# Optimization experiments

Measured on AMD Instinct MI355X. Metric: run time of the kernel, lower is better.

The kernel has to match this reference:

```python
import jax, jax.numpy as jnp
import numpy as np

D_MODEL, D_STATE, D_CONV, EXPAND = 1024, 16, 4, 2
D_INNER = EXPAND * D_MODEL
BATCH, SEQ = 2, 2048


def setup_inputs() -> dict:
    key = jax.random.key(0)
    ks = jax.random.split(key, 10)
    s = lambda fan_in: 1.0 / np.sqrt(fan_in)
    return {
        "x": jax.random.normal(ks[0], (BATCH, SEQ, D_MODEL), jnp.float32),
        "W_in": jax.random.normal(ks[1], (2 * D_INNER, D_MODEL), jnp.float32) * s(D_MODEL),
        "w_conv": jax.random.normal(ks[2], (D_INNER, D_CONV), jnp.float32) * s(D_CONV),
        "b_conv": jax.random.normal(ks[3], (D_INNER,), jnp.float32) * 0.02,
        "W_x": jax.random.normal(ks[4], (D_INNER + 2 * D_STATE, D_INNER), jnp.float32) * s(D_INNER),
        "W_dt": jax.random.normal(ks[5], (D_INNER, D_INNER), jnp.float32) * s(D_INNER),
        "b_dt": jax.random.normal(ks[6], (D_INNER,), jnp.float32) * 0.02,
        "A_log": jnp.log(jax.random.uniform(ks[7], (D_INNER, D_STATE), jnp.float32, 1e-4, 1.0)),
        "D": jnp.ones((D_INNER,), jnp.float32),
        "W_out": jax.random.normal(ks[8], (D_MODEL, D_INNER), jnp.float32) * s(D_INNER),
    }


def _depthwise_causal_conv(x, w, b):
    # x: (B, L, C), w: (C, K), causal (left-pad K-1), matches conv1d(padding=K-1)[..., :L]
    K = w.shape[1]
    L = x.shape[1]
    xp = jnp.pad(x, ((0, 0), (K - 1, 0), (0, 0)))
    out = b
    for k in range(K):  # K is tiny (4)
        out = out + xp[:, k:k + L, :] * w[:, k]
    return out


def _selective_scan(x, delta, Bm, Cm, A, Dv):
    # x, delta: (B, L, d_inner); Bm, Cm: (B, L, d_state)
    def step(state, inp):
        x_t, d_t, B_t, C_t = inp  # (B,d_inner),(B,d_inner),(B,d_state),(B,d_state)
        decay = jnp.exp(d_t[..., None] * A)          # (B, d_inner, d_state)
        state = decay * state + B_t[:, None, :] * x_t[..., None]
        y_t = jnp.einsum('bds,bs->bd', state, C_t) + x_t * Dv
        return state, y_t

    init = jnp.zeros((x.shape[0], x.shape[2], A.shape[1]), x.dtype)
    xs = tuple(jnp.swapaxes(a, 0, 1) for a in (x, delta, Bm, Cm))
    _, ys = jax.lax.scan(step, init, xs)             # ys: (L, B, d_inner)
    return jnp.swapaxes(ys, 0, 1)


def reference(x, W_in, w_conv, b_conv, W_x, W_dt, b_dt, A_log, D, W_out):
    silu = jax.nn.silu
    xz = x @ W_in.T                                   # (B, L, 2*d_inner)
    x_inner, z = jnp.split(xz, 2, axis=-1)
    x_conv = silu(_depthwise_causal_conv(x_inner, w_conv, b_conv))
    x_dbl = x_conv @ W_x.T                            # (B, L, d_inner + 2*d_state)
    delta, Bm, Cm = jnp.split(x_dbl, [D_INNER, D_INNER + D_STATE], axis=-1)
    delta = jax.nn.softplus(delta @ W_dt.T + b_dt)
    A = -jnp.exp(A_log.astype(jnp.float32))
    y = _selective_scan(x_conv, delta, Bm, Cm, A, D)
    y = y * silu(z)
    return y @ W_out.T
```

## Files before the change

### kernel.cpp

```cpp
#include <hip/hip_runtime.h>
#include <hip/hip_bf16.h>


#define BATCH 2
#define SEQ   2048
#define DM    1024
#define DI    2048
#define DS    16
#define T_TOK (BATCH * SEQ)

#define CL 64
#define NC 32

typedef __bf16 v8bf __attribute__((ext_vector_type(8)));
typedef float  v4f  __attribute__((ext_vector_type(4)));

__device__ __forceinline__ void gld16(const void* g, void* l) {
    __builtin_amdgcn_global_load_lds(
        (const __attribute__((address_space(1))) void*)g,
        (__attribute__((address_space(3))) void*)l, 16, 0, 0);
}

__device__ __forceinline__ float b2f(__hip_bfloat16 v) { return __bfloat162float(v); }

__device__ __forceinline__ int is_bf(const void* Dref) {
    return ((const unsigned*)Dref)[0] == 0x3F803F80u;
}

__device__ __forceinline__ float load_in(const void* p, size_t i, int isbf) {
    return isbf ? b2f(((const __hip_bfloat16*)p)[i]) : ((const float*)p)[i];
}

__device__ __forceinline__ float softplus_f(float x) {
    return (x > 15.f) ? x : __logf(1.f + __expf(x));
}

#define NBIG0 (T_TOK * DM)
#define NBIG1 (4096 * DM)
#define NBIG2 (DI * DI)
#define NBIG3 (DM * DI)
#define NB_BIG 7168
#define NB_TR  1024
#define NB_SM  184
#define NB_PAD 128
#define NB_ALL (NB_BIG + NB_TR + NB_SM + NB_PAD)

__global__ __launch_bounds__(256) void convert_all(
    const void* __restrict__ s0, const void* __restrict__ s1,
    const void* __restrict__ s2, const void* __restrict__ s3,
    __hip_bfloat16* __restrict__ d0, __hip_bfloat16* __restrict__ d1,
    __hip_bfloat16* __restrict__ d2, __hip_bfloat16* __restrict__ d3,
    const void* __restrict__ wconv, const void* __restrict__ bconv,
    const void* __restrict__ bdt, const void* __restrict__ dv,
    const void* __restrict__ A_log,
    __hip_bfloat16* __restrict__ wconvb, __hip_bfloat16* __restrict__ bconvb,
    __hip_bfloat16* __restrict__ bdtb, __hip_bfloat16* __restrict__ db,
    float* __restrict__ Amat,
    const void* __restrict__ Wx, __hip_bfloat16* __restrict__ WxdT,
    __hip_bfloat16* __restrict__ Wxp)
{
    __shared__ __bf16 t[64][72];
    const int isbf = is_bf(dv);
    const int bid = blockIdx.x;

    if (bid < NB_BIG) {
        if (isbf) return;
        size_t e = ((size_t)bid * 256 + threadIdx.x) * 8;
        const float* src; __hip_bfloat16* dst;
        if (e < NBIG0)                      { src = (const float*)s0 + e;                 dst = d0 + e; }
        else if (e < NBIG0 + NBIG1)         { e -= NBIG0; src = (const float*)s1 + e;     dst = d1 + e; }
        else if (e < NBIG0 + NBIG1 + NBIG2) { e -= NBIG0 + NBIG1; src = (const float*)s2 + e; dst = d2 + e; }
        else                                { e -= NBIG0 + NBIG1 + NBIG2; src = (const float*)s3 + e; dst = d3 + e; }
        const float4 a = *(const float4*)src;
        const float4 b = *(const float4*)(src + 4);
        __bf16 o[8] = {(__bf16)a.x,(__bf16)a.y,(__bf16)a.z,(__bf16)a.w,
                       (__bf16)b.x,(__bf16)b.y,(__bf16)b.z,(__bf16)b.w};
        *(uint4*)dst = *(uint4*)&o[0];
    } else if (bid < NB_BIG + NB_TR) {
        const int b2 = bid - NB_BIG;
        const int bi = (b2 >> 5) * 64;
        const int bj = (b2 & 31) * 64;
        const int rr = threadIdx.x >> 3;
        const int c0 = (threadIdx.x & 7) * 8;
#pragma unroll
        for (int k = 0; k < 2; k++) {
            const int r = rr + k * 32;
            const size_t src = (size_t)(bi + r) * DI + bj + c0;
            __bf16 o[8];
            if (isbf) {
                *(uint4*)&o[0] = *(const uint4*)((const __hip_bfloat16*)Wx + src);
            } else {
                const float* s = (const float*)Wx + src;
                const float4 a = *(const float4*)s;
                const float4 b = *(const float4*)(s + 4);
                o[0]=(__bf16)a.x; o[1]=(__bf16)a.y; o[2]=(__bf16)a.z; o[3]=(__bf16)a.w;
                o[4]=(__bf16)b.x; o[5]=(__bf16)b.y; o[6]=(__bf16)b.z; o[7]=(__bf16)b.w;
            }
            *(uint4*)&t[r][c0] = *(uint4*)&o[0];
        }
        __syncthreads();
#pragma unroll
        for (int k = 0; k < 2; k++) {
            const int dr = rr + k * 32;
            __bf16 o[8];
#pragma unroll
            for (int j = 0; j < 8; j++) o[j] = t[c0 + j][dr];
            *(uint4*)(WxdT + (size_t)(bj + dr) * DI + bi + c0) = *(uint4*)&o[0];
        }
    } else if (bid < NB_BIG + NB_TR + NB_SM) {
        const int i = (bid - (NB_BIG + NB_TR)) * 256 + threadIdx.x;
        if (i < 8192)        wconvb[i]        = __float2bfloat16(load_in(wconv, i, isbf));
        else if (i < 10240)  bconvb[i - 8192] = __float2bfloat16(load_in(bconv, i - 8192, isbf));
        else if (i < 12288)  bdtb[i - 10240]  = __float2bfloat16(load_in(bdt, i - 10240, isbf));
        else if (i < 14336)  db[i - 12288]    = __float2bfloat16(load_in(dv, i - 12288, isbf));
        else if (i < 47104)  Amat[i - 14336]  = -__expf(load_in(A_log, i - 14336, isbf));
    } else {
        const size_t e = ((size_t)(bid - (NB_BIG + NB_TR + NB_SM)) * 256 + threadIdx.x) * 8;
        if (e >= (size_t)128 * DI) return;
        const size_t base = (size_t)2048 * DI;
        if (e >= (size_t)32 * DI) {
            __bf16 z[8] = {};
            *(uint4*)(Wxp + base + e) = *(uint4*)&z[0];
            return;
        }
        if (isbf) {
            *(uint4*)(Wxp + base + e) = *(const uint4*)((const __hip_bfloat16*)Wx + base + e);
        } else {
            const float* src = (const float*)Wx + base + e;
            const float4 a = *(const float4*)src;
            const float4 b = *(const float4*)(src + 4);
            __bf16 o[8] = {(__bf16)a.x,(__bf16)a.y,(__bf16)a.z,(__bf16)a.w,
                           (__bf16)b.x,(__bf16)b.y,(__bf16)b.z,(__bf16)b.w};
            *(uint4*)(Wxp + base + e) = *(uint4*)&o[0];
        }
    }
}

template <int MODE, int TN>
__device__ __forceinline__ void gemm_core(
    const __hip_bfloat16* __restrict__ A, const __hip_bfloat16* __restrict__ Bw,
    void* __restrict__ out0, void* __restrict__ out1,
    int isbf, int id, int nx, int nblk, int N, int K)
{
    constexpr int NF = TN / 32;
    constexpr int ASLOT = 512;
    constexpr int BSLOT = TN * 4;
    __shared__ v8bf Asv[2 * ASLOT];
    __shared__ v8bf Bsv[2 * BSLOT];

    const int sid = (id & 7) * (nblk >> 3) + (id >> 3);
    const int bxs = sid % nx;
    const int bys = sid / nx;

    const int tid  = threadIdx.x;
    const int bm   = bys * 128;
    const int bn   = bxs * TN;
    const int w    = tid >> 6;
    const int lane = tid & 63;
    const int wm   = (w >> 1) * 64;
    const int wn   = (w & 1) * (TN / 2);
    const int lrow  = lane & 15;
    const int lquad = lane >> 4;

    v4f acc[4][NF];
#pragma unroll
    for (int i = 0; i < 4; i++)
#pragma unroll
        for (int j = 0; j < NF; j++) acc[i][j] = (v4f){0.f, 0.f, 0.f, 0.f};

    const int r0 = tid >> 2;
    const int q0 = (tid & 3) ^ ((r0 >> 1) & 3);
    const __hip_bfloat16* gA0 = A  + (size_t)(bm + r0) * K + q0 * 8;
    const __hip_bfloat16* gA1 = A  + (size_t)(bm + 64 + r0) * K + q0 * 8;
    const __hip_bfloat16* gB0 = Bw + (size_t)(bn + r0) * K + q0 * 8;
    const __hip_bfloat16* gB1 = Bw + (size_t)(bn + 64 + r0) * K + q0 * 8;
    char* lA0 = (char*)Asv + tid * 16;
    char* lA1 = (char*)Asv + 4096 + tid * 16;
    char* lB0 = (char*)Bsv + tid * 16;
    char* lB1 = (char*)Bsv + 4096 + tid * 16;

    const int swz = lquad ^ ((lrow >> 1) & 3);
    int sA[4], sB[NF];
#pragma unroll
    for (int i = 0; i < 4; i++) sA[i] = (wm + i * 16 + lrow) * 4 + swz;
#pragma unroll
    for (int i = 0; i < NF; i++) sB[i] = (wn + i * 16 + lrow) * 4 + swz;

    const int NIT = K >> 5;
    gld16(gA0, lA0);
    gld16(gA1, lA1);
    gld16(gB0, lB0);
    if (TN == 128) gld16(gB1, lB1);

    int k = 32;
    for (int it = 0; it < NIT; ++it) {
        const int cb = it & 1;
        __syncthreads();
        if (it + 1 < NIT) {
            const int pa = (cb ^ 1) * 8192;
            const int pb = (cb ^ 1) * (BSLOT * 16);
            gld16(gA0 + k, lA0 + pa);
            gld16(gA1 + k, lA1 + pa);
            gld16(gB0 + k, lB0 + pb);
            if (TN == 128) gld16(gB1 + k, lB1 + pb);
            k += 32;
        }
        const int ca = cb * ASLOT;
        const int cbb = cb * BSLOT;
        v8bf af[4], bfr[NF];
#pragma unroll
        for (int i = 0; i < 4; i++)
            af[i] = Asv[ca + sA[i]];
#pragma unroll
        for (int i = 0; i < NF; i++)
            bfr[i] = Bsv[cbb + sB[i]];
#pragma unroll
        for (int mi = 0; mi < 4; mi++)
#pragma unroll
            for (int ni = 0; ni < NF; ni++)
                acc[mi][ni] = __builtin_amdgcn_mfma_f32_16x16x32_bf16(
                    af[mi], bfr[ni], acc[mi][ni], 0, 0, 0);
    }

#pragma unroll
    for (int mi = 0; mi < 4; mi++) {
#pragma unroll
        for (int ni = 0; ni < NF; ni++) {
#pragma unroll
            for (int r = 0; r < 4; r++) {
                const int grow = bm + wm + mi * 16 + lquad * 4 + r;
                const int gcol = bn + wn + ni * 16 + lrow;
                const float v = acc[mi][ni][r];
                if (MODE == 0) {
                    ((__hip_bfloat16*)out0)[(size_t)grow * N + gcol] = __float2bfloat16(v);
                } else if (MODE == 1) {
                    if (gcol < 2048) {
                        ((__hip_bfloat16*)out0)[(size_t)grow * 2048 + gcol] = __float2bfloat16(v);
                    } else if (gcol < 2080) {
                        ((float*)out1)[(size_t)grow * 32 + (gcol - 2048)] = v;
                    }
                } else {
                    if (isbf)
                        ((__hip_bfloat16*)out0)[(size_t)grow * N + gcol] = __float2bfloat16(v);
                    else
                        ((float*)out0)[(size_t)grow * N + gcol] = v;
                }
            }
        }
    }
}

template <int MODE, int TN>
__global__ __launch_bounds__(256) void gemm_single(
    const __hip_bfloat16* __restrict__ Ac, const void* __restrict__ Araw,
    const __hip_bfloat16* __restrict__ Bc, const void* __restrict__ Braw,
    void* __restrict__ out0, void* __restrict__ out1,
    const void* __restrict__ Dref, int N, int K)
{
    const int isbf = is_bf(Dref);
    const __hip_bfloat16* A = (isbf && Araw) ? (const __hip_bfloat16*)Araw : Ac;
    const __hip_bfloat16* B = (isbf && Braw) ? (const __hip_bfloat16*)Braw : Bc;
    const int nx = gridDim.x;
    const int nblk = gridDim.x * gridDim.y;
    const int id = blockIdx.y * nx + blockIdx.x;
    gemm_core<MODE, TN>(A, B, out0, out1, isbf, id, nx, nblk, N, K);
}

__global__ __launch_bounds__(256) void gemm_dual(
    const __hip_bfloat16* __restrict__ A1c, const void* __restrict__ A1raw,
    const __hip_bfloat16* __restrict__ B1c, const void* __restrict__ B1raw,
    void* __restrict__ o1,
    const __hip_bfloat16* __restrict__ A2c, const void* __restrict__ A2raw,
    const __hip_bfloat16* __restrict__ B2,
    void* __restrict__ o2,
    const void* __restrict__ Dref)
{
    const int isbf = is_bf(Dref);
    if (blockIdx.x < 1024) {
        const __hip_bfloat16* A = (isbf && A1raw) ? (const __hip_bfloat16*)A1raw : A1c;
        const __hip_bfloat16* B = (isbf && B1raw) ? (const __hip_bfloat16*)B1raw : B1c;
        gemm_core<0, 128>(A, B, o1, nullptr, isbf, blockIdx.x, 32, 1024, 4096, 1024);
    } else {
        const __hip_bfloat16* A = (isbf && A2raw) ? (const __hip_bfloat16*)A2raw : A2c;
        gemm_core<0, 128>(A, B2, o2, nullptr, isbf, blockIdx.x - 1024, 16, 256, 2048, 2048);
    }
}

__global__ __launch_bounds__(256) void conv_silu(
    const __hip_bfloat16* __restrict__ xz,
    const __hip_bfloat16* __restrict__ wconv,
    const __hip_bfloat16* __restrict__ bconv,
    __hip_bfloat16* __restrict__ xconv)
{
    const int idx = blockIdx.x * 256 + threadIdx.x;
    const int c8 = (idx & 255) << 3;
    const int tg = idx >> 8;
    const int tl = tg & (SEQ - 1);

    __bf16 wl[32], bl[8];
    *(uint4*)&wl[0]  = *(const uint4*)(wconv + c8 * 4);
    *(uint4*)&wl[8]  = *(const uint4*)(wconv + c8 * 4 + 8);
    *(uint4*)&wl[16] = *(const uint4*)(wconv + c8 * 4 + 16);
    *(uint4*)&wl[24] = *(const uint4*)(wconv + c8 * 4 + 24);
    *(uint4*)&bl[0]  = *(const uint4*)(bconv + c8);

    float acc[8];
#pragma unroll
    for (int cc = 0; cc < 8; cc++) acc[cc] = (float)bl[cc];

#pragma unroll
    for (int k = 0; k < 4; k++) {
        const int ts = tl - 3 + k;
        if (ts >= 0) {
            __bf16 xl[8];
            *(uint4*)&xl[0] = *(const uint4*)(xz + (size_t)(tg - 3 + k) * 4096 + c8);
#pragma unroll
            for (int cc = 0; cc < 8; cc++)
                acc[cc] += (float)wl[cc * 4 + k] * (float)xl[cc];
        }
    }

    __bf16 o[8];
#pragma unroll
    for (int cc = 0; cc < 8; cc++) {
        const float s = acc[cc] / (1.f + __expf(-acc[cc]));
        o[cc] = (__bf16)s;
    }
    *(uint4*)(xconv + (size_t)tg * DI + c8) = *(uint4*)&o[0];
}

__global__ __launch_bounds__(256) void scan_p1(
    const __hip_bfloat16* __restrict__ dlin, const __hip_bfloat16* __restrict__ xconv,
    const float* __restrict__ BCg, const float* __restrict__ Amat,
    const __hip_bfloat16* __restrict__ bdt,
    float* __restrict__ Pws, float* __restrict__ Sws)
{
    const int d = blockIdx.x * 256 + threadIdx.x;
    const int c = blockIdx.y;
    const int b = blockIdx.z;
    const int tg0 = b * SEQ + c * CL;

    __shared__ float bc[CL * 32];
    for (int i = threadIdx.x; i < CL * 32; i += 256) bc[i] = BCg[(size_t)tg0 * 32 + i];
    __syncthreads();

    float Areg[DS];
#pragma unroll
    for (int s = 0; s < DS; s++) Areg[s] = Amat[d * DS + s];
    const float bd = b2f(bdt[d]);

    float P[DS], S[DS];
#pragma unroll
    for (int s = 0; s < DS; s++) { P[s] = 1.f; S[s] = 0.f; }

    for (int i = 0; i < CL; i++) {
        const size_t tg = tg0 + i;
        const float dl = softplus_f(b2f(dlin[tg * DI + d]) + bd);
        const float x  = b2f(xconv[tg * DI + d]);
#pragma unroll
        for (int s = 0; s < DS; s++) {
            const float e = __expf(dl * Areg[s]);
            P[s] *= e;
            S[s] = e * S[s] + bc[i * 32 + s] * x;
        }
    }

    const size_t base = (((size_t)b * NC + c) * DI + d) * DS;
#pragma unroll
    for (int s = 0; s < DS; s += 4) {
        *(float4*)(Pws + base + s) = make_float4(P[s], P[s+1], P[s+2], P[s+3]);
        *(float4*)(Sws + base + s) = make_float4(S[s], S[s+1], S[s+2], S[s+3]);
    }
}

__global__ void scan_p2(float* __restrict__ Pws, float* __restrict__ Sws) {
    const int idx = blockIdx.x * 256 + threadIdx.x;
    const int b  = idx >> 15;
    const int ds = idx & 32767;
    float carry = 0.f;
    for (int c = 0; c < NC; c++) {
        const size_t a = (((size_t)b * NC + c) << 15) + ds;
        const float p  = Pws[a];
        const float sv = Sws[a];
        Sws[a] = carry;
        carry = p * carry + sv;
    }
}

__global__ __launch_bounds__(256) void scan_p3(
    const __hip_bfloat16* __restrict__ dlin, const __hip_bfloat16* __restrict__ xconv,
    const float* __restrict__ BCg, const float* __restrict__ Amat,
    const __hip_bfloat16* __restrict__ bdt,
    const float* __restrict__ Sws, const __hip_bfloat16* __restrict__ xz,
    const __hip_bfloat16* __restrict__ Dv, __hip_bfloat16* __restrict__ yg)
{
    const int d = blockIdx.x * 256 + threadIdx.x;
    const int c = blockIdx.y;
    const int b = blockIdx.z;
    const int tg0 = b * SEQ + c * CL;

    __shared__ float bc[CL * 32];
    for (int i = threadIdx.x; i < CL * 32; i += 256) bc[i] = BCg[(size_t)tg0 * 32 + i];
    __syncthreads();

    float Areg[DS];
#pragma unroll
    for (int s = 0; s < DS; s++) Areg[s] = Amat[d * DS + s];
    const float bd = b2f(bdt[d]);

    const size_t base = (((size_t)b * NC + c) * DI + d) * DS;
    float S[DS];
#pragma unroll
    for (int s = 0; s < DS; s += 4) {
        const float4 v = *(const float4*)(Sws + base + s);
        S[s] = v.x; S[s+1] = v.y; S[s+2] = v.z; S[s+3] = v.w;
    }
    const float Dd = b2f(Dv[d]);

    for (int i = 0; i < CL; i++) {
        const size_t tg = tg0 + i;
        const float dl = softplus_f(b2f(dlin[tg * DI + d]) + bd);
        const float x  = b2f(xconv[tg * DI + d]);
        float y = 0.f;
#pragma unroll
        for (int s = 0; s < DS; s++) {
            const float e = __expf(dl * Areg[s]);
            S[s] = e * S[s] + bc[i * 32 + s] * x;
            y += S[s] * bc[i * 32 + 16 + s];
        }
        y += x * Dd;
        const float z = b2f(xz[tg * 4096 + 2048 + d]);
        const float g = z / (1.f + __expf(-z));
        yg[tg * DI + d] = __float2bfloat16(y * g);
    }
}

extern "C" void kernel_launch(void* const* d_in, const int* in_sizes, int n_in,
                              void* d_out, int out_size, void* d_ws, size_t ws_size,
                              hipStream_t stream)
{
    const void* x_raw     = d_in[0];
    const void* W_in_raw  = d_in[1];
    const void* wconv_raw = d_in[2];
    const void* bconv_raw = d_in[3];
    const void* W_x_raw   = d_in[4];
    const void* W_dt_raw  = d_in[5];
    const void* b_dt_raw  = d_in[6];
    const void* A_log_raw = d_in[7];
    const void* D_raw     = d_in[8];
    const void* W_out_raw = d_in[9];

    char* ws = (char*)d_ws;
    size_t off = 0;
    auto alloc = [&](size_t bytes) { char* p = ws + off; off += (bytes + 255) & ~(size_t)255; return p; };
    __hip_bfloat16* XB    = (__hip_bfloat16*)alloc((size_t)T_TOK * DM * 2);
    __hip_bfloat16* WINB  = (__hip_bfloat16*)alloc((size_t)4096 * DM * 2);
    __hip_bfloat16* WDTB  = (__hip_bfloat16*)alloc((size_t)DI * DI * 2);
    __hip_bfloat16* WOUTB = (__hip_bfloat16*)alloc((size_t)DM * DI * 2);
    __hip_bfloat16* WCONVB= (__hip_bfloat16*)alloc((size_t)DI * 4 * 2);
    __hip_bfloat16* BCONVB= (__hip_bfloat16*)alloc((size_t)DI * 2);
    __hip_bfloat16* BDTB  = (__hip_bfloat16*)alloc((size_t)DI * 2);
    __hip_bfloat16* DB    = (__hip_bfloat16*)alloc((size_t)DI * 2);
    __hip_bfloat16* XZ    = (__hip_bfloat16*)alloc((size_t)T_TOK * 4096 * 2);
    __hip_bfloat16* XCONV = (__hip_bfloat16*)alloc((size_t)T_TOK * DI * 2);
    __hip_bfloat16* WXDT  = (__hip_bfloat16*)alloc((size_t)DI * DI * 2);
    __hip_bfloat16* WXPAD = (__hip_bfloat16*)alloc((size_t)2176 * DI * 2);
    float*          BC    = (float*)alloc((size_t)T_TOK * 32 * 4);
    __hip_bfloat16* DELTA = (__hip_bfloat16*)alloc((size_t)T_TOK * DI * 2);
    float*          AMAT  = (float*)alloc((size_t)DI * DS * 4);
    float*          PWS   = (float*)alloc((size_t)BATCH * NC * DI * DS * 4);
    float*          SWS   = (float*)alloc((size_t)BATCH * NC * DI * DS * 4);
    __hip_bfloat16* YG    = (__hip_bfloat16*)alloc((size_t)T_TOK * DI * 2);

    convert_all<<<NB_ALL, 256, 0, stream>>>(
        x_raw, W_in_raw, W_dt_raw, W_out_raw, XB, WINB, WDTB, WOUTB,
        wconv_raw, bconv_raw, b_dt_raw, D_raw, A_log_raw,
        WCONVB, BCONVB, BDTB, DB, AMAT,
        W_x_raw, WXDT, WXPAD);

    gemm_dual<<<1280, 256, 0, stream>>>(
        XB, x_raw, WINB, W_in_raw, XZ,
        WDTB, W_dt_raw, WXDT, WXPAD, D_raw);

    conv_silu<<<T_TOK, 256, 0, stream>>>(XZ, WCONVB, BCONVB, XCONV);

    gemm_single<1, 128><<<dim3(17, 32), 256, 0, stream>>>(
        XCONV, nullptr, WXPAD, nullptr, DELTA, BC, D_raw, 2176, 2048);

    scan_p1<<<dim3(DI / 256, NC, BATCH), 256, 0, stream>>>(
        DELTA, XCONV, BC, AMAT, BDTB, PWS, SWS);
    scan_p2<<<(BATCH * DI * DS) / 256, 256, 0, stream>>>(PWS, SWS);
    scan_p3<<<dim3(DI / 256, NC, BATCH), 256, 0, stream>>>(
        DELTA, XCONV, BC, AMAT, BDTB, SWS, XZ, DB, YG);

    gemm_single<3, 128><<<dim3(8, 32), 256, 0, stream>>>(
        YG, nullptr, WOUTB, W_out_raw, d_out, nullptr, D_raw, 1024, 2048);
}
```

Measured before the change: 458.4 us.

## Fold log2e into A, reuse conv rows, remap GEMM tiles per XCD, narrow out-proj tile

Scales A by log2(e) at conversion time so the scan kernels can use exp2f in place of __expf, which saves a multiply per state element. The conv+SiLU kernel now produces four tokens per thread from seven loaded rows, so overlapping inputs are reused and a quarter as many blocks are launched. The GEMM block-to-tile mapping gives each XCD a contiguous 2D patch when the grid divides evenly, aiming at better L2 locality. The output projection uses 64-wide N tiles to double the block count, at the cost of less reuse per block.

```diff
diff --git a/kernel.cpp b/kernel.cpp
--- a/kernel.cpp
+++ b/kernel.cpp
@@ -44,6 +44,8 @@
 #define NB_SM  184
 #define NB_PAD 128
 #define NB_ALL (NB_BIG + NB_TR + NB_SM + NB_PAD)
+
+#define LOG2E 1.44269504088896340736f
 
 __global__ __launch_bounds__(256) void convert_all(
     const void* __restrict__ s0, const void* __restrict__ s1,
@@ -113,7 +115,7 @@
         else if (i < 10240)  bconvb[i - 8192] = __float2bfloat16(load_in(bconv, i - 8192, isbf));
         else if (i < 12288)  bdtb[i - 10240]  = __float2bfloat16(load_in(bdt, i - 10240, isbf));
         else if (i < 14336)  db[i - 12288]    = __float2bfloat16(load_in(dv, i - 12288, isbf));
-        else if (i < 47104)  Amat[i - 14336]  = -__expf(load_in(A_log, i - 14336, isbf));
+        else if (i < 47104)  Amat[i - 14336]  = -__expf(load_in(A_log, i - 14336, isbf)) * LOG2E;
     } else {
         const size_t e = ((size_t)(bid - (NB_BIG + NB_TR + NB_SM)) * 256 + threadIdx.x) * 8;
         if (e >= (size_t)128 * DI) return;
@@ -148,9 +150,18 @@
     __shared__ v8bf Asv[2 * ASLOT];
     __shared__ v8bf Bsv[2 * BSLOT];
 
-    const int sid = (id & 7) * (nblk >> 3) + (id >> 3);
-    const int bxs = sid % nx;
-    const int bys = sid / nx;
+    const int ny = nblk / nx;
+    int bxs, bys;
+    if (((nx & 3) == 0) && ((ny & 1) == 0)) {
+        const int rx = nx >> 2, ry = ny >> 1;
+        const int xcd = id & 7, lid = id >> 3;
+        bxs = (xcd & 3) * rx + lid % rx;
+        bys = (xcd >> 2) * ry + lid / rx;
+    } else {
+        const int sid = (id & 7) * (nblk >> 3) + (id >> 3);
+        bxs = sid % nx;
+        bys = sid / nx;
+    }
 
     const int tid  = threadIdx.x;
     const int bm   = bys * 128;
@@ -293,9 +304,10 @@
     __hip_bfloat16* __restrict__ xconv)
 {
     const int idx = blockIdx.x * 256 + threadIdx.x;
-    const int c8 = (idx & 255) << 3;
-    const int tg = idx >> 8;
-    const int tl = tg & (SEQ - 1);
+    const int c8  = (idx & 255) << 3;
+    const int g   = idx >> 8;
+    const int tg0 = g << 2;
+    const int tl0 = tg0 & (SEQ - 1);
 
     __bf16 wl[32], bl[8];
     *(uint4*)&wl[0]  = *(const uint4*)(wconv + c8 * 4);
@@ -304,29 +316,38 @@
     *(uint4*)&wl[24] = *(const uint4*)(wconv + c8 * 4 + 24);
     *(uint4*)&bl[0]  = *(const uint4*)(bconv + c8);
 
-    float acc[8];
-#pragma unroll
-    for (int cc = 0; cc < 8; cc++) acc[cc] = (float)bl[cc];
-
-#pragma unroll
-    for (int k = 0; k < 4; k++) {
-        const int ts = tl - 3 + k;
-        if (ts >= 0) {
-            __bf16 xl[8];
-            *(uint4*)&xl[0] = *(const uint4*)(xz + (size_t)(tg - 3 + k) * 4096 + c8);
+    __bf16 rows[7][8];
+#pragma unroll
+    for (int j = 0; j < 7; j++) {
+        const int ts = tl0 - 3 + j;
+        if (ts >= 0 && j < 3) {
+            *(uint4*)&rows[j][0] = *(const uint4*)(xz + (size_t)(tg0 - 3 + j) * 4096 + c8);
+        } else if (j >= 3) {
+            *(uint4*)&rows[j][0] = *(const uint4*)(xz + (size_t)(tg0 - 3 + j) * 4096 + c8);
+        } else {
+            __bf16 z[8] = {};
+            *(uint4*)&rows[j][0] = *(uint4*)&z[0];
+        }
+    }
+
+#pragma unroll
+    for (int i = 0; i < 4; i++) {
+        float acc[8];
+#pragma unroll
+        for (int cc = 0; cc < 8; cc++) acc[cc] = (float)bl[cc];
+#pragma unroll
+        for (int k = 0; k < 4; k++)
 #pragma unroll
             for (int cc = 0; cc < 8; cc++)
-                acc[cc] += (float)wl[cc * 4 + k] * (float)xl[cc];
-        }
-    }
-
-    __bf16 o[8];
-#pragma unroll
-    for (int cc = 0; cc < 8; cc++) {
-        const float s = acc[cc] / (1.f + __expf(-acc[cc]));
-        o[cc] = (__bf16)s;
-    }
-    *(uint4*)(xconv + (size_t)tg * DI + c8) = *(uint4*)&o[0];
+                acc[cc] += (float)wl[cc * 4 + k] * (float)rows[i + k][cc];
+        __bf16 o[8];
+#pragma unroll
+        for (int cc = 0; cc < 8; cc++) {
+            const float s = acc[cc] / (1.f + __expf(-acc[cc]));
+            o[cc] = (__bf16)s;
+        }
+        *(uint4*)(xconv + (size_t)(tg0 + i) * DI + c8) = *(uint4*)&o[0];
+    }
 }
 
 __global__ __launch_bounds__(256) void scan_p1(
@@ -359,7 +380,7 @@
         const float x  = b2f(xconv[tg * DI + d]);
 #pragma unroll
         for (int s = 0; s < DS; s++) {
-            const float e = __expf(dl * Areg[s]);
+            const float e = exp2f(dl * Areg[s]);
             P[s] *= e;
             S[s] = e * S[s] + bc[i * 32 + s] * x;
         }
@@ -424,7 +445,7 @@
         float y = 0.f;
 #pragma unroll
         for (int s = 0; s < DS; s++) {
-            const float e = __expf(dl * Areg[s]);
+            const float e = exp2f(dl * Areg[s]);
             S[s] = e * S[s] + bc[i * 32 + s] * x;
             y += S[s] * bc[i * 32 + 16 + s];
         }
@@ -482,7 +503,7 @@
         XB, x_raw, WINB, W_in_raw, XZ,
         WDTB, W_dt_raw, WXDT, WXPAD, D_raw);
 
-    conv_silu<<<T_TOK, 256, 0, stream>>>(XZ, WCONVB, BCONVB, XCONV);
+    conv_silu<<<T_TOK / 4, 256, 0, stream>>>(XZ, WCONVB, BCONVB, XCONV);
 
     gemm_single<1, 128><<<dim3(17, 32), 256, 0, stream>>>(
         XCONV, nullptr, WXPAD, nullptr, DELTA, BC, D_raw, 2176, 2048);
@@ -493,6 +514,6 @@
     scan_p3<<<dim3(DI / 256, NC, BATCH), 256, 0, stream>>>(
         DELTA, XCONV, BC, AMAT, BDTB, SWS, XZ, DB, YG);
 
-    gemm_single<3, 128><<<dim3(8, 32), 256, 0, stream>>>(
+    gemm_single<3, 64><<<dim3(16, 32), 256, 0, stream>>>(
         YG, nullptr, WOUTB, W_out_raw, d_out, nullptr, D_raw, 1024, 2048);
 }
```

Measured after the change: 445.7 us. 2.8% less time.
